# Optimization experiments

Measured on AMD Instinct MI355X. Metric: run time of the kernel, lower is better.

## Reference

```python
import jax, jax.numpy as jnp
import numpy as np

REG = 0.01
MAX_ITER = 200


def setup_inputs() -> dict:
    key = jax.random.key(0)
    kA, kB = jax.random.split(key)
    N, D = 8192, 768
    A = jax.random.normal(kA, (N, D), dtype=jnp.float32)
    B = jax.random.normal(kB, (N, D), dtype=jnp.float32)
    return {"A": A, "B": B}


def _cdist(A, B):
    # Euclidean pairwise distances [N, M] via the Gram trick.
    sqA = jnp.sum(A * A, axis=1, keepdims=True)          # [N,1]
    sqB = jnp.sum(B * B, axis=1, keepdims=True).T        # [1,M]
    sq = sqA + sqB - 2.0 * (A @ B.T)
    return jnp.sqrt(jnp.maximum(sq, 0.0))


def _sinkhorn(M, reg, max_iter):
    # POT ot.sinkhorn with a = b = ones(N) (unnormalized uniform marginals),
    # implemented in the numerically-equivalent log domain for fp32 stability
    # (POT runs the naive scaling loop in float64 numpy on CPU).
    n, m = M.shape
    logK = -M / reg                                      # [N,M]
    # u0 = 1/n, v0 = 1/m  ->  f0 = -log n, g0 = -log m
    f0 = jnp.full((n,), -jnp.log(jnp.asarray(n, M.dtype)), M.dtype)
    g0 = jnp.full((m,), -jnp.log(jnp.asarray(m, M.dtype)), M.dtype)

    def body(i, fg):
        f, g = fg
        # v = b / (K^T u)  with b = 1  ->  g = -logsumexp(logK + f, axis=0)
        g = -jax.nn.logsumexp(logK + f[:, None], axis=0)
        # u = a / (K v)    with a = 1  ->  f = -logsumexp(logK + g, axis=1)
        f = -jax.nn.logsumexp(logK + g[None, :], axis=1)
        return (f, g)

    f, g = jax.lax.fori_loop(0, max_iter, body, (f0, g0))
    return jnp.exp(logK + f[:, None] + g[None, :])       # T = diag(u) K diag(v)


def reference(A, B):
    # compute_distance_matrix: cdist -> clamp(1e-6) -> / max
    dist = _cdist(A, B)
    dist = jnp.maximum(dist, 1e-6)
    dist = dist / jnp.max(dist)
    # forward: extra clamp(1e-6)
    dist = jnp.maximum(dist, 1e-6)
    # transport matrix is computed on detached numpy in the original -> constant
    T = jax.lax.stop_gradient(_sinkhorn(dist, REG, MAX_ITER))
    aligned_A = T @ A
    aligned_B = T.T @ B
    return (aligned_A, aligned_B)
```

## Files before the change

kernel.cpp:

```cpp
#include <hip/hip_runtime.h>
#include <stdint.h>

#define NN 8192
#define DD 768
#define LOG2E 1.4426950408889634f

typedef unsigned int  U32;
typedef unsigned short U16;
typedef __attribute__((ext_vector_type(8))) short short8;
typedef __attribute__((ext_vector_type(4))) float f32x4;

__device__ __forceinline__ U32 fkey(float x){
  U32 u = __float_as_uint(x);
  return (u & 0x80000000u) ? ~u : (u | 0x80000000u);
}
__device__ __forceinline__ float funkey(U32 k){
  return __uint_as_float((k & 0x80000000u) ? (k ^ 0x80000000u) : ~k);
}
__device__ __forceinline__ float ex2(float x){ return __builtin_amdgcn_exp2f(x); }
__device__ __forceinline__ float rcpf(float x){ return __builtin_amdgcn_rcpf(x); }
__device__ __forceinline__ float bflo(U32 w){ return __uint_as_float(w << 16); }
__device__ __forceinline__ float bfhi(U32 w){ return __uint_as_float(w & 0xFFFF0000u); }
__device__ __forceinline__ U16 tobf(float x){
  U32 a = __float_as_uint(x);
  return (U16)((a + 0x7FFFu + ((a >> 16) & 1u)) >> 16);
}
__device__ __forceinline__ U32 packbf(float lo, float hi){
  U32 a = __float_as_uint(lo), b = __float_as_uint(hi);
  a = a + 0x7FFFu + ((a >> 16) & 1u);
  b = b + 0x7FFFu + ((b >> 16) & 1u);
  return (a >> 16) | (b & 0xFFFF0000u);
}

__global__ __launch_bounds__(64) void k_init(U32* slots){
  if (threadIdx.x == 0){ slots[0]=0u; slots[1]=0xFFFFFFFFu; slots[2]=0u; slots[3]=0u; }
}

__global__ __launch_bounds__(256) void k_sqsum(const float* __restrict__ A, const float* __restrict__ B,
                                               float* sqA, float* sqB, U32* slots){
  int wv = threadIdx.x >> 6, ln = threadIdx.x & 63;
  int row = blockIdx.x*4 + wv;
  const float* src = A; float* dst = sqA; U32* slot = slots + 2; int r = row;
  if (row >= NN){ src = B; dst = sqB; slot = slots + 3; r = row - NN; }
  const float* p = src + (size_t)r * DD;
  float s = 0.f;
  #pragma unroll
  for (int m = 0; m < DD/64; ++m){ float v = p[ln + 64*m]; s = fmaf(v, v, s); }
  #pragma unroll
  for (int o = 32; o; o >>= 1) s += __shfl_xor(s, o);
  if (ln == 0){ dst[r] = s; atomicMax(slot, fkey(s)); }
}

__global__ __launch_bounds__(256) void k_dist(const float* __restrict__ A, const float* __restrict__ B,
                                              U16* __restrict__ q, const float* __restrict__ sqA,
                                              const float* __restrict__ sqB, U32* slots){
  __shared__ float As[16][128], Bs[16][128];
  __shared__ U32 redmx[4], redmn[4];
  const int t = threadIdx.x;
  const int i0 = blockIdx.y*128, j0 = blockIdx.x*128;
  const float S = 65535.f / (sqrtf(funkey(slots[2])) + sqrtf(funkey(slots[3])));
  float acc[8][8];
  #pragma unroll
  for (int m=0;m<8;m++)
    #pragma unroll
    for (int n=0;n<8;n++) acc[m][n] = 0.f;
  const int lr = t >> 1, lk = (t & 1)*8;
  const float* pa = A + (size_t)(i0+lr)*DD + lk;
  const float* pb = B + (size_t)(j0+lr)*DD + lk;
  const int tx = t & 15, ty = t >> 4;
  for (int k0 = 0; k0 < DD; k0 += 16){
    __syncthreads();
    float4 a0 = *(const float4*)(pa + k0);
    float4 a1 = *(const float4*)(pa + k0 + 4);
    float4 b0 = *(const float4*)(pb + k0);
    float4 b1 = *(const float4*)(pb + k0 + 4);
    As[lk+0][lr]=a0.x; As[lk+1][lr]=a0.y; As[lk+2][lr]=a0.z; As[lk+3][lr]=a0.w;
    As[lk+4][lr]=a1.x; As[lk+5][lr]=a1.y; As[lk+6][lr]=a1.z; As[lk+7][lr]=a1.w;
    Bs[lk+0][lr]=b0.x; Bs[lk+1][lr]=b0.y; Bs[lk+2][lr]=b0.z; Bs[lk+3][lr]=b0.w;
    Bs[lk+4][lr]=b1.x; Bs[lk+5][lr]=b1.y; Bs[lk+6][lr]=b1.z; Bs[lk+7][lr]=b1.w;
    __syncthreads();
    #pragma unroll
    for (int kk = 0; kk < 16; ++kk){
      float4 am0 = *(const float4*)&As[kk][ty*8];
      float4 am1 = *(const float4*)&As[kk][ty*8+4];
      float4 bn0 = *(const float4*)&Bs[kk][tx*8];
      float4 bn1 = *(const float4*)&Bs[kk][tx*8+4];
      float ar[8] = {am0.x,am0.y,am0.z,am0.w,am1.x,am1.y,am1.z,am1.w};
      float br[8] = {bn0.x,bn0.y,bn0.z,bn0.w,bn1.x,bn1.y,bn1.z,bn1.w};
      #pragma unroll
      for (int m=0;m<8;m++)
        #pragma unroll
        for (int n=0;n<8;n++) acc[m][n] = fmaf(ar[m], br[n], acc[m][n]);
    }
  }
  U32 bmax = 0u, bmin = 0xFFFFu;
  #pragma unroll
  for (int m=0;m<8;m++){
    int i = i0 + ty*8 + m;
    float sa = sqA[i];
    U16 pk[8] __attribute__((aligned(16)));
    #pragma unroll
    for (int n=0;n<8;n++){
      int j = j0 + tx*8 + n;
      float sq = sa + sqB[j] - 2.f*acc[m][n];
      float d = sqrtf(fmaxf(sq, 0.f));
      d = fmaxf(d, 1e-6f);
      U32 qv = (U32)rintf(d * S);
      if (qv > 65535u) qv = 65535u;
      bmax = bmax > qv ? bmax : qv;
      bmin = bmin < qv ? bmin : qv;
      pk[n] = (U16)qv;
    }
    *(uint4*)(q + (size_t)i*NN + j0 + tx*8) = *(const uint4*)pk;
  }
  #pragma unroll
  for (int o=32;o;o>>=1){
    U32 om = __shfl_xor(bmax, o); bmax = bmax > om ? bmax : om;
    U32 on = __shfl_xor(bmin, o); bmin = bmin < on ? bmin : on;
  }
  if ((t & 63) == 0){ redmx[t>>6] = bmax; redmn[t>>6] = bmin; }
  __syncthreads();
  if (t == 0){
    U32 mx = redmx[0], mn = redmn[0];
    #pragma unroll
    for (int i=1;i<4;i++){ mx = mx > redmx[i] ? mx : redmx[i]; mn = mn < redmn[i] ? mn : redmn[i]; }
    atomicMax(slots+0, mx); atomicMin(slots+1, mn);
  }
}

__global__ __launch_bounds__(256) void k_buildK(U32* K2, const U32* __restrict__ slots){
  const float qmaxf = (float)slots[0];
  const float r0n = (float)slots[1] / qmaxf;
  const float k1 = -100.f*LOG2E/qmaxf;
  const float c2 = 50.f*(1.f + r0n)*LOG2E;
  const float tcl = -1e-4f*LOG2E;
  size_t base = ((size_t)blockIdx.x*256 + threadIdx.x)*4;
  uint4 w = *(uint4*)(K2 + base);
  U32 r[4];
  U32 in[4] = {w.x, w.y, w.z, w.w};
  #pragma unroll
  for (int k=0;k<4;++k){
    float ql = (float)(in[k] & 0xFFFFu);
    float qh = (float)(in[k] >> 16);
    float el = ex2(fminf(ql*k1, tcl) + c2);
    float eh = ex2(fminf(qh*k1, tcl) + c2);
    r[k] = packbf(el, eh);
  }
  *(uint4*)(K2 + base) = make_uint4(r[0], r[1], r[2], r[3]);
}

template<int FIRST>
__global__ __launch_bounds__(256) void k_fused(const uint4* __restrict__ Kp,
                                               const float* __restrict__ v,
                                               float* __restrict__ u,
                                               U32* __restrict__ partb){
  __shared__ float4 vl4[2048];
  __shared__ float ws[2][4][4];
  const int t = threadIdx.x;
  const int rc = blockIdx.x;
  const int r0 = rc*8;
  const int wv = t >> 6, ln = t & 63;
  if (!FIRST){
    #pragma unroll
    for (int h = 0; h < 8; ++h){
      int V = t + 256*h;
      vl4[V ^ ((V >> 3) & 7)] = ((const float4*)v)[V];
    }
    __syncthreads();
  }
  float a[4][8];
  #pragma unroll
  for (int s=0;s<4;++s)
    #pragma unroll
    for (int e=0;e<8;++e) a[s][e] = 0.f;

  #pragma unroll
  for (int g=0; g<2; ++g){
    uint4 kw[4][4];
    #pragma unroll
    for (int rr=0; rr<4; ++rr)
      #pragma unroll
      for (int s=0; s<4; ++s)
        kw[rr][s] = Kp[(size_t)(r0 + g*4 + rr)*1024 + s*256 + t];
    float uu[4];
    if (!FIRST){
      float d[4] = {0.f,0.f,0.f,0.f};
      #pragma unroll
      for (int s=0; s<4; ++s){
        int V = (s*256 + t)*2;
        int msk = (V >> 3) & 7;
        float4 v0 = vl4[V ^ msk];
        float4 v1 = vl4[(V + 1) ^ msk];
        #pragma unroll
        for (int rr=0; rr<4; ++rr){
          uint4 w = kw[rr][s];
          d[rr]=fmaf(bflo(w.x),v0.x,d[rr]); d[rr]=fmaf(bfhi(w.x),v0.y,d[rr]);
          d[rr]=fmaf(bflo(w.y),v0.z,d[rr]); d[rr]=fmaf(bfhi(w.y),v0.w,d[rr]);
          d[rr]=fmaf(bflo(w.z),v1.x,d[rr]); d[rr]=fmaf(bfhi(w.z),v1.y,d[rr]);
          d[rr]=fmaf(bflo(w.w),v1.z,d[rr]); d[rr]=fmaf(bfhi(w.w),v1.w,d[rr]);
        }
      }
      #pragma unroll
      for (int o=32; o; o>>=1){
        #pragma unroll
        for (int rr=0; rr<4; ++rr) d[rr] += __shfl_xor(d[rr], o);
      }
      if (ln == 0){
        #pragma unroll
        for (int rr=0; rr<4; ++rr) ws[g & 1][rr][wv] = d[rr];
      }
      __syncthreads();
      #pragma unroll
      for (int rr=0; rr<4; ++rr)
        uu[rr] = rcpf(ws[g&1][rr][0] + ws[g&1][rr][1] + ws[g&1][rr][2] + ws[g&1][rr][3]);
    } else {
      #pragma unroll
      for (int rr=0; rr<4; ++rr) uu[rr] = 1.0f/8192.0f;
    }
    if (t < 4) u[r0 + g*4 + t] = uu[t];
    #pragma unroll
    for (int rr=0; rr<4; ++rr){
      float ur = uu[rr];
      #pragma unroll
      for (int s=0; s<4; ++s){
        uint4 w = kw[rr][s];
        a[s][0]=fmaf(bflo(w.x),ur,a[s][0]); a[s][1]=fmaf(bfhi(w.x),ur,a[s][1]);
        a[s][2]=fmaf(bflo(w.y),ur,a[s][2]); a[s][3]=fmaf(bfhi(w.y),ur,a[s][3]);
        a[s][4]=fmaf(bflo(w.z),ur,a[s][4]); a[s][5]=fmaf(bfhi(w.z),ur,a[s][5]);
        a[s][6]=fmaf(bflo(w.w),ur,a[s][6]); a[s][7]=fmaf(bfhi(w.w),ur,a[s][7]);
      }
    }
  }
  #pragma unroll
  for (int s=0; s<4; ++s){
    U32* pp = partb + (size_t)rc*4096 + (s*256 + t)*4;
    *(uint4*)pp = make_uint4(packbf(a[s][0],a[s][1]), packbf(a[s][2],a[s][3]),
                             packbf(a[s][4],a[s][5]), packbf(a[s][6],a[s][7]));
  }
}

__global__ __launch_bounds__(256) void k_vfin(const U32* __restrict__ partb, float* __restrict__ v){
  __shared__ float red[16][16][2];
  const int t = threadIdx.x;
  const int pr = t & 15, kk = t >> 4;
  const int cw = blockIdx.x*16 + pr;
  float s0 = 0.f, s1 = 0.f;
  #pragma unroll 8
  for (int m = 0; m < 64; ++m){
    U32 w = partb[(size_t)(kk*64 + m)*4096 + cw];
    s0 += bflo(w); s1 += bfhi(w);
  }
  red[pr][kk][0] = s0; red[pr][kk][1] = s1;
  __syncthreads();
  if (t < 32){
    int p2 = t >> 1, hf = t & 1;
    float s = 0.f;
    #pragma unroll
    for (int k=0;k<16;++k) s += red[p2][k][hf];
    v[blockIdx.x*32 + p2*2 + hf] = rcpf(s);
  }
}

__global__ __launch_bounds__(256) void k_At(const float* __restrict__ X, const float* __restrict__ sc,
                                            U16* __restrict__ Xth, U16* __restrict__ Xtl){
  __shared__ float Ts[64][65];
  const int t = threadIdx.x;
  const int d0 = blockIdx.x*64, j0 = blockIdx.y*64;
  {
    const int r = t >> 2, cs = (t & 3)*16;
    const float vj = sc[j0 + r];
    #pragma unroll
    for (int e=0;e<4;++e){
      float4 a4 = *(const float4*)(X + (size_t)(j0+r)*DD + d0 + cs + e*4);
      Ts[r][cs+e*4+0]=a4.x*vj; Ts[r][cs+e*4+1]=a4.y*vj;
      Ts[r][cs+e*4+2]=a4.z*vj; Ts[r][cs+e*4+3]=a4.w*vj;
    }
  }
  __syncthreads();
  {
    const int dr = t >> 2, jseg = t & 3;
    U16 hh[16], ll[16];
    #pragma unroll
    for (int e=0;e<16;++e){
      float x = Ts[jseg*16+e][dr];
      U16 h = tobf(x);
      hh[e] = h;
      ll[e] = tobf(x - __uint_as_float(((U32)h) << 16));
    }
    size_t off = (size_t)(d0+dr)*NN + j0 + jseg*16;
    *(uint4*)(Xth + off)     = *(const uint4*)&hh[0];
    *(uint4*)(Xth + off + 8) = *(const uint4*)&hh[8];
    *(uint4*)(Xtl + off)     = *(const uint4*)&ll[0];
    *(uint4*)(Xtl + off + 8) = *(const uint4*)&ll[8];
  }
}

__global__ __launch_bounds__(512) void k_outA(const U16* __restrict__ Kp,
                                              const U16* __restrict__ Ath, const U16* __restrict__ Atl,
                                              const float* __restrict__ u, float* __restrict__ outA){
  __shared__ U16 Ks[128][40];
  __shared__ U16 Ah[192][40];
  __shared__ U16 Al[192][40];
  const int t = threadIdx.x;
  const int i0 = blockIdx.y*128, d0 = blockIdx.x*192;
  const int w  = t >> 6, lane = t & 63;
  const int wm = w >> 1, wn = w & 1;
  const int l15 = lane & 15, lhi = lane >> 4;
  f32x4 acc[2][6];
  #pragma unroll
  for (int fm=0;fm<2;++fm)
    #pragma unroll
    for (int fn=0;fn<6;++fn) acc[fm][fn] = (f32x4){0.f,0.f,0.f,0.f};

  const int sr = t >> 2, sseg = t & 3;
  for (int j0 = 0; j0 < NN; j0 += 32){
    __syncthreads();
    {
      uint4 kw = *(const uint4*)(Kp + (size_t)(i0+sr)*NN + j0 + sseg*8);
      *(uint4*)&Ks[sr][sseg*8] = kw;
      #pragma unroll
      for (int uu=0; uu<3; ++uu){
        int id = t + 512*uu;
        if (id < 768){
          int r = id >> 2, seg = id & 3;
          uint4 aw = *(const uint4*)(Ath + (size_t)(d0+r)*NN + j0 + seg*8);
          *(uint4*)&Ah[r][seg*8] = aw;
        } else {
          int rid = id - 768;
          int r = rid >> 2, seg = rid & 3;
          uint4 aw = *(const uint4*)(Atl + (size_t)(d0+r)*NN + j0 + seg*8);
          *(uint4*)&Al[r][seg*8] = aw;
        }
      }
    }
    __syncthreads();
    short8 af[2];
    #pragma unroll
    for (int fm=0;fm<2;++fm)
      af[fm] = *(const short8*)&Ks[wm*32 + fm*16 + l15][lhi*8];
    #pragma unroll
    for (int fn=0;fn<6;++fn){
      short8 bh = *(const short8*)&Ah[wn*96 + fn*16 + l15][lhi*8];
      short8 bl = *(const short8*)&Al[wn*96 + fn*16 + l15][lhi*8];
      #pragma unroll
      for (int fm=0;fm<2;++fm){
        acc[fm][fn] = __builtin_amdgcn_mfma_f32_16x16x32_bf16(af[fm], bh, acc[fm][fn], 0, 0, 0);
        acc[fm][fn] = __builtin_amdgcn_mfma_f32_16x16x32_bf16(af[fm], bl, acc[fm][fn], 0, 0, 0);
      }
    }
  }
  float us[2][4];
  #pragma unroll
  for (int fm=0;fm<2;++fm)
    #pragma unroll
    for (int r=0;r<4;++r) us[fm][r] = u[i0 + wm*32 + fm*16 + lhi*4 + r];
  #pragma unroll
  for (int fm=0;fm<2;++fm)
    #pragma unroll
    for (int fn=0;fn<6;++fn)
      #pragma unroll
      for (int r=0;r<4;++r){
        int i = i0 + wm*32 + fm*16 + lhi*4 + r;
        int d = d0 + wn*96 + fn*16 + l15;
        outA[(size_t)i*DD + d] = acc[fm][fn][r] * us[fm][r];
      }
}

__global__ __launch_bounds__(512) void k_outBm(const U16* __restrict__ Kp,
                                               const U16* __restrict__ Bth, const U16* __restrict__ Btl,
                                               const float* __restrict__ v, float* __restrict__ outB){
  __shared__ U16 Kt[128][40];
  __shared__ U16 Bh[192][40];
  __shared__ U16 Bl[192][40];
  const int t = threadIdx.x;
  const int j0 = blockIdx.y*128, d0 = blockIdx.x*192;
  const int w  = t >> 6, lane = t & 63;
  const int wm = w >> 1, wn = w & 1;
  const int l15 = lane & 15, lhi = lane >> 4;
  f32x4 acc[2][6];
  #pragma unroll
  for (int fm=0;fm<2;++fm)
    #pragma unroll
    for (int fn=0;fn<6;++fn) acc[fm][fn] = (f32x4){0.f,0.f,0.f,0.f};

  const int i_l = t & 31, jseg = t >> 5;
  for (int i0k = 0; i0k < NN; i0k += 32){
    __syncthreads();
    {
      uint4 kw = *(const uint4*)(Kp + (size_t)(i0k+i_l)*NN + j0 + jseg*8);
      const U16* pk = (const U16*)&kw;
      #pragma unroll
      for (int e=0;e<8;++e) Kt[jseg*8+e][i_l] = pk[e];
      #pragma unroll
      for (int uu=0; uu<3; ++uu){
        int id = t + 512*uu;
        if (id < 768){
          int r = id >> 2, seg = id & 3;
          uint4 bw = *(const uint4*)(Bth + (size_t)(d0+r)*NN + i0k + seg*8);
          *(uint4*)&Bh[r][seg*8] = bw;
        } else {
          int rid = id - 768;
          int r = rid >> 2, seg = rid & 3;
          uint4 bw = *(const uint4*)(Btl + (size_t)(d0+r)*NN + i0k + seg*8);
          *(uint4*)&Bl[r][seg*8] = bw;
        }
      }
    }
    __syncthreads();
    short8 af[2];
    #pragma unroll
    for (int fm=0;fm<2;++fm)
      af[fm] = *(const short8*)&Kt[wm*32 + fm*16 + l15][lhi*8];
    #pragma unroll
    for (int fn=0;fn<6;++fn){
      short8 bh = *(const short8*)&Bh[wn*96 + fn*16 + l15][lhi*8];
      short8 bl = *(const short8*)&Bl[wn*96 + fn*16 + l15][lhi*8];
      #pragma unroll
      for (int fm=0;fm<2;++fm){
        acc[fm][fn] = __builtin_amdgcn_mfma_f32_16x16x32_bf16(af[fm], bh, acc[fm][fn], 0, 0, 0);
        acc[fm][fn] = __builtin_amdgcn_mfma_f32_16x16x32_bf16(af[fm], bl, acc[fm][fn], 0, 0, 0);
      }
    }
  }
  float vs[2][4];
  #pragma unroll
  for (int fm=0;fm<2;++fm)
    #pragma unroll
    for (int r=0;r<4;++r) vs[fm][r] = v[j0 + wm*32 + fm*16 + lhi*4 + r];
  #pragma unroll
  for (int fm=0;fm<2;++fm)
    #pragma unroll
    for (int fn=0;fn<6;++fn)
      #pragma unroll
      for (int r=0;r<4;++r){
        int j = j0 + wm*32 + fm*16 + lhi*4 + r;
        int d = d0 + wn*96 + fn*16 + l15;
        outB[(size_t)j*DD + d] = acc[fm][fn][r] * vs[fm][r];
      }
}

extern "C" void kernel_launch(void* const* d_in, const int* in_sizes, int n_in,
                              void* d_out, int out_size, void* d_ws, size_t ws_size,
                              hipStream_t stream) {
  const float* A = (const float*)d_in[0];
  const float* B = (const float*)d_in[1];
  float* out = (float*)d_out;
  char* ws = (char*)d_ws;
  U16*  q     = (U16*) (ws);
  float* u    = (float*)(ws + 136314880);
  float* v    = (float*)(ws + 136347648);
  float* sqA  = (float*)(ws + 136380416);
  float* sqB  = (float*)(ws + 136413184);
  U32*  slots = (U32*) (ws + 136445952);
  U32*  partb = (U32*) (ws + 136511552);
  U16* Bth = (U16*)(ws + 136511552);
  U16* Btl = Bth + (size_t)NN*DD;
  U16* Ath = (U16*)(out + (size_t)NN*DD);
  U16* Atl = Ath + (size_t)NN*DD;

  k_init<<<1, 64, 0, stream>>>(slots);
  k_sqsum<<<4096, 256, 0, stream>>>(A, B, sqA, sqB, slots);
  k_dist<<<dim3(64,64), 256, 0, stream>>>(A, B, q, sqA, sqB, slots);
  k_buildK<<<32768, 256, 0, stream>>>((U32*)q, slots);

  const uint4* Kp4 = (const uint4*)q;
  k_fused<1><<<1024, 256, 0, stream>>>(Kp4, v, u, partb);
  for (int it = 0; it < 200; ++it){
    k_vfin<<<256, 256, 0, stream>>>(partb, v);
    k_fused<0><<<1024, 256, 0, stream>>>(Kp4, v, u, partb);
  }

  k_At<<<dim3(12,128), 256, 0, stream>>>(A, v, Ath, Atl);
  k_outA<<<dim3(4,64), 512, 0, stream>>>(q, Ath, Atl, u, out);
  k_At<<<dim3(12,128), 256, 0, stream>>>(B, u, Bth, Btl);
  k_outBm<<<dim3(4,64), 512, 0, stream>>>(q, Bth, Btl, v, out + (size_t)NN*DD);
}
```

Baseline: 9.498 ms.

## Compute distance Gram with split-bf16 MFMA and keep v in registers

Replaces the scalar fp32 FMA tiled distance GEMM with a 512-thread kernel that splits A and B into bf16 hi/lo parts and uses three bf16 MFMA products per tile to approximate fp32 accuracy. This targets the cost of an 8192x8192x768 GEMM run on vector ALUs. Separately, the Sinkhorn fused kernel now loads its slice of v straight into registers instead of staging the whole vector through swizzled shared memory with a barrier. The epilogue now writes the quantized distances as scattered 16-bit stores instead of packed 16-byte stores. The hi/lo split drops the lo*lo term, which risks small precision loss in the distances.

```diff
diff --git a/kernel.cpp b/kernel.cpp
--- a/kernel.cpp
+++ b/kernel.cpp
@@ -51,79 +51,100 @@
   if (ln == 0){ dst[r] = s; atomicMax(slot, fkey(s)); }
 }
 
-__global__ __launch_bounds__(256) void k_dist(const float* __restrict__ A, const float* __restrict__ B,
-                                              U16* __restrict__ q, const float* __restrict__ sqA,
-                                              const float* __restrict__ sqB, U32* slots){
-  __shared__ float As[16][128], Bs[16][128];
-  __shared__ U32 redmx[4], redmn[4];
+__global__ __launch_bounds__(512) void k_distm(const float* __restrict__ A, const float* __restrict__ B,
+                                               U16* __restrict__ q, const float* __restrict__ sqA,
+                                               const float* __restrict__ sqB, U32* slots){
+  __shared__ U16 Ahs[128][40], Als[128][40];
+  __shared__ U16 Bhs[128][40], Bls[128][40];
+  __shared__ U32 redmx[8], redmn[8];
   const int t = threadIdx.x;
   const int i0 = blockIdx.y*128, j0 = blockIdx.x*128;
   const float S = 65535.f / (sqrtf(funkey(slots[2])) + sqrtf(funkey(slots[3])));
-  float acc[8][8];
-  #pragma unroll
-  for (int m=0;m<8;m++)
-    #pragma unroll
-    for (int n=0;n<8;n++) acc[m][n] = 0.f;
-  const int lr = t >> 1, lk = (t & 1)*8;
-  const float* pa = A + (size_t)(i0+lr)*DD + lk;
-  const float* pb = B + (size_t)(j0+lr)*DD + lk;
-  const int tx = t & 15, ty = t >> 4;
-  for (int k0 = 0; k0 < DD; k0 += 16){
-    __syncthreads();
-    float4 a0 = *(const float4*)(pa + k0);
-    float4 a1 = *(const float4*)(pa + k0 + 4);
-    float4 b0 = *(const float4*)(pb + k0);
-    float4 b1 = *(const float4*)(pb + k0 + 4);
-    As[lk+0][lr]=a0.x; As[lk+1][lr]=a0.y; As[lk+2][lr]=a0.z; As[lk+3][lr]=a0.w;
-    As[lk+4][lr]=a1.x; As[lk+5][lr]=a1.y; As[lk+6][lr]=a1.z; As[lk+7][lr]=a1.w;
-    Bs[lk+0][lr]=b0.x; Bs[lk+1][lr]=b0.y; Bs[lk+2][lr]=b0.z; Bs[lk+3][lr]=b0.w;
-    Bs[lk+4][lr]=b1.x; Bs[lk+5][lr]=b1.y; Bs[lk+6][lr]=b1.z; Bs[lk+7][lr]=b1.w;
-    __syncthreads();
-    #pragma unroll
-    for (int kk = 0; kk < 16; ++kk){
-      float4 am0 = *(const float4*)&As[kk][ty*8];
-      float4 am1 = *(const float4*)&As[kk][ty*8+4];
-      float4 bn0 = *(const float4*)&Bs[kk][tx*8];
-      float4 bn1 = *(const float4*)&Bs[kk][tx*8+4];
-      float ar[8] = {am0.x,am0.y,am0.z,am0.w,am1.x,am1.y,am1.z,am1.w};
-      float br[8] = {bn0.x,bn0.y,bn0.z,bn0.w,bn1.x,bn1.y,bn1.z,bn1.w};
-      #pragma unroll
-      for (int m=0;m<8;m++)
-        #pragma unroll
-        for (int n=0;n<8;n++) acc[m][n] = fmaf(ar[m], br[n], acc[m][n]);
+  const int w = t >> 6, lane = t & 63;
+  const int wm = w >> 1, wn = w & 1;
+  const int l15 = lane & 15, lhi = lane >> 4;
+  f32x4 acc[2][4];
+  #pragma unroll
+  for (int fm=0;fm<2;++fm)
+    #pragma unroll
+    for (int fn=0;fn<4;++fn) acc[fm][fn] = (f32x4){0.f,0.f,0.f,0.f};
+
+  const int sr = t >> 2, sseg = t & 3;
+  for (int k0 = 0; k0 < DD; k0 += 32){
+    __syncthreads();
+    {
+      const float* pa = A + (size_t)(i0+sr)*DD + k0 + sseg*8;
+      const float* pb = B + (size_t)(j0+sr)*DD + k0 + sseg*8;
+      float4 a0 = *(const float4*)pa;
+      float4 a1 = *(const float4*)(pa+4);
+      float4 b0 = *(const float4*)pb;
+      float4 b1 = *(const float4*)(pb+4);
+      float av[8] = {a0.x,a0.y,a0.z,a0.w,a1.x,a1.y,a1.z,a1.w};
+      float bv[8] = {b0.x,b0.y,b0.z,b0.w,b1.x,b1.y,b1.z,b1.w};
+      U16 ah[8], al[8], bh[8], bl[8];
+      #pragma unroll
+      for (int e=0;e<8;++e){
+        U16 h = tobf(av[e]); ah[e] = h;
+        al[e] = tobf(av[e] - __uint_as_float(((U32)h)<<16));
+        U16 g = tobf(bv[e]); bh[e] = g;
+        bl[e] = tobf(bv[e] - __uint_as_float(((U32)g)<<16));
+      }
+      *(uint4*)&Ahs[sr][sseg*8] = *(const uint4*)ah;
+      *(uint4*)&Als[sr][sseg*8] = *(const uint4*)al;
+      *(uint4*)&Bhs[sr][sseg*8] = *(const uint4*)bh;
+      *(uint4*)&Bls[sr][sseg*8] = *(const uint4*)bl;
+    }
+    __syncthreads();
+    short8 fah[2], fal[2];
+    #pragma unroll
+    for (int fm=0;fm<2;++fm){
+      fah[fm] = *(const short8*)&Ahs[wm*32 + fm*16 + l15][lhi*8];
+      fal[fm] = *(const short8*)&Als[wm*32 + fm*16 + l15][lhi*8];
+    }
+    #pragma unroll
+    for (int fn=0;fn<4;++fn){
+      short8 fbh = *(const short8*)&Bhs[wn*64 + fn*16 + l15][lhi*8];
+      short8 fbl = *(const short8*)&Bls[wn*64 + fn*16 + l15][lhi*8];
+      #pragma unroll
+      for (int fm=0;fm<2;++fm){
+        acc[fm][fn] = __builtin_amdgcn_mfma_f32_16x16x32_bf16(fah[fm], fbh, acc[fm][fn], 0, 0, 0);
+        acc[fm][fn] = __builtin_amdgcn_mfma_f32_16x16x32_bf16(fah[fm], fbl, acc[fm][fn], 0, 0, 0);
+        acc[fm][fn] = __builtin_amdgcn_mfma_f32_16x16x32_bf16(fal[fm], fbh, acc[fm][fn], 0, 0, 0);
+      }
     }
   }
   U32 bmax = 0u, bmin = 0xFFFFu;
   #pragma unroll
-  for (int m=0;m<8;m++){
-    int i = i0 + ty*8 + m;
-    float sa = sqA[i];
-    U16 pk[8] __attribute__((aligned(16)));
-    #pragma unroll
-    for (int n=0;n<8;n++){
-      int j = j0 + tx*8 + n;
-      float sq = sa + sqB[j] - 2.f*acc[m][n];
-      float d = sqrtf(fmaxf(sq, 0.f));
-      d = fmaxf(d, 1e-6f);
-      U32 qv = (U32)rintf(d * S);
-      if (qv > 65535u) qv = 65535u;
-      bmax = bmax > qv ? bmax : qv;
-      bmin = bmin < qv ? bmin : qv;
-      pk[n] = (U16)qv;
-    }
-    *(uint4*)(q + (size_t)i*NN + j0 + tx*8) = *(const uint4*)pk;
+  for (int fm=0;fm<2;++fm){
+    #pragma unroll
+    for (int fn=0;fn<4;++fn){
+      int j = j0 + wn*64 + fn*16 + l15;
+      float sb = sqB[j];
+      #pragma unroll
+      for (int r=0;r<4;++r){
+        int i = i0 + wm*32 + fm*16 + lhi*4 + r;
+        float sq = sqA[i] + sb - 2.f*acc[fm][fn][r];
+        float d = sqrtf(fmaxf(sq, 0.f));
+        d = fmaxf(d, 1e-6f);
+        U32 qv = (U32)rintf(d * S);
+        if (qv > 65535u) qv = 65535u;
+        bmax = bmax > qv ? bmax : qv;
+        bmin = bmin < qv ? bmin : qv;
+        q[(size_t)i*NN + j] = (U16)qv;
+      }
+    }
   }
   #pragma unroll
   for (int o=32;o;o>>=1){
     U32 om = __shfl_xor(bmax, o); bmax = bmax > om ? bmax : om;
     U32 on = __shfl_xor(bmin, o); bmin = bmin < on ? bmin : on;
   }
-  if ((t & 63) == 0){ redmx[t>>6] = bmax; redmn[t>>6] = bmin; }
+  if (lane == 0){ redmx[w] = bmax; redmn[w] = bmin; }
   __syncthreads();
   if (t == 0){
     U32 mx = redmx[0], mn = redmn[0];
     #pragma unroll
-    for (int i=1;i<4;i++){ mx = mx > redmx[i] ? mx : redmx[i]; mn = mn < redmn[i] ? mn : redmn[i]; }
+    for (int i=1;i<8;i++){ mx = mx > redmx[i] ? mx : redmx[i]; mn = mn < redmn[i] ? mn : redmn[i]; }
     atomicMax(slots+0, mx); atomicMin(slots+1, mn);
   }
 }
@@ -154,19 +175,18 @@
                                                const float* __restrict__ v,
                                                float* __restrict__ u,
                                                U32* __restrict__ partb){
-  __shared__ float4 vl4[2048];
   __shared__ float ws[2][4][4];
   const int t = threadIdx.x;
   const int rc = blockIdx.x;
   const int r0 = rc*8;
   const int wv = t >> 6, ln = t & 63;
+  float4 vr[4][2];
   if (!FIRST){
     #pragma unroll
-    for (int h = 0; h < 8; ++h){
-      int V = t + 256*h;
-      vl4[V ^ ((V >> 3) & 7)] = ((const float4*)v)[V];
-    }
-    __syncthreads();
+    for (int s=0;s<4;++s){
+      vr[s][0] = *(const float4*)(v + s*2048 + t*8);
+      vr[s][1] = *(const float4*)(v + s*2048 + t*8 + 4);
+    }
   }
   float a[4][8];
   #pragma unroll
@@ -187,10 +207,8 @@
       float d[4] = {0.f,0.f,0.f,0.f};
       #pragma unroll
       for (int s=0; s<4; ++s){
-        int V = (s*256 + t)*2;
-        int msk = (V >> 3) & 7;
-        float4 v0 = vl4[V ^ msk];
-        float4 v1 = vl4[(V + 1) ^ msk];
+        float4 v0 = vr[s][0];
+        float4 v1 = vr[s][1];
         #pragma unroll
         for (int rr=0; rr<4; ++rr){
           uint4 w = kw[rr][s];
@@ -460,7 +478,7 @@
 
   k_init<<<1, 64, 0, stream>>>(slots);
   k_sqsum<<<4096, 256, 0, stream>>>(A, B, sqA, sqB, slots);
-  k_dist<<<dim3(64,64), 256, 0, stream>>>(A, B, q, sqA, sqB, slots);
+  k_distm<<<dim3(64,64), 512, 0, stream>>>(A, B, q, sqA, sqB, slots);
   k_buildK<<<32768, 256, 0, stream>>>((U32*)q, slots);
 
   const uint4* Kp4 = (const uint4*)q;
```

Result: faster. 8.685 ms (median of 2 runs) (-8.6%).
